# Performance work log

Measured on AMD Instinct MI355X. Metric: run time of the kernel, lower is better.

The kernel has to match this reference:

```python
import jax, jax.numpy as jnp
import numpy as np

ANG_Y, ANG_X = 3, 3
ST = ANG_Y * ANG_X
K = 9                      # square kernel
OH, OW = 128, 128          # output_size
IN_C, OUT_C = 3, 3
H, W = 384, 384
B = 4


def setup_inputs() -> dict:
    key = jax.random.key(0)
    k_lf, = jax.random.split(key, 1)
    lf = jax.random.uniform(k_lf, (B, ST, IN_C, H, W), dtype=jnp.float32)
    # Learned locally-connected weights: one (out_c, in_c, OH, OW, K*K) tensor
    # per angular position, initialized as the center-tap identity (as in __init__).
    weights = jnp.zeros((ST, OUT_C, IN_C, OH, OW, K * K), dtype=jnp.float32)
    center = (K * K) // 2
    ch = jnp.arange(IN_C)
    weights = weights.at[:, ch, ch, :, :, center].set(1.0)
    biases = jnp.zeros((ST, OUT_C, OH, OW), dtype=jnp.float32)
    return {"lf": lf, "weights": weights, "biases": biases}


def reference(lf, weights, biases):
    b, st, c, h, w = lf.shape
    dh, dw = ANG_Y, ANG_X  # unfold stride
    # Padding exactly as in linear_filter
    pad_x = (OW - 1) * ANG_X + (K - w)
    pad_right = pad_x // 2
    pad_left = pad_x - pad_right
    pad_y = (OH - 1) * ANG_Y + (K - h)
    pad_bottom = pad_y // 2
    pad_top = pad_y - pad_bottom
    padded = jnp.pad(
        lf, ((0, 0), (0, 0), (0, 0), (pad_top, pad_bottom), (pad_left, pad_right))
    )
    # Extract K x K windows with stride (dh, dw), vectorized over batch and
    # all angular positions at once (replaces the triple Python loop).
    rows = jnp.arange(OH) * dh          # (OH,)
    cols = jnp.arange(OW) * dw          # (OW,)
    koff = jnp.arange(K)                # (K,)
    p = padded[:, :, :, rows[:, None] + koff[None, :], :]          # (b,st,c,OH,K,Wp)
    p = p[:, :, :, :, :, cols[:, None] + koff[None, :]]            # (b,st,c,OH,K,OW,K)
    p = p.transpose(0, 1, 2, 3, 5, 4, 6).reshape(b, st, c, OH, OW, K * K)
    # Locally-connected (unshared-weight) conv: per-angular, per-pixel weights.
    out = jnp.einsum("bsihwk,soihwk->bsohw", p, weights) + biases[None]
    return jnp.clip(out, 0.0, 1.0)
```

## Files before the change

### kernel.cpp

```cpp
#include <hip/hip_runtime.h>


#define ST 9
#define INC 3
#define OUTC 3
#define OHH 128
#define OWW 128
#define KDIM 9
#define KK 81
#define HH 384
#define WW 384
#define HWSZ (HH*WW)
#define WQ 32
#define SLICE (WQ*KK)

typedef float f32x4 __attribute__((ext_vector_type(4)));
struct __attribute__((packed, aligned(4))) U4 { f32x4 v; };

__device__ __forceinline__ void gll16(const float* g, float* l) {
  __builtin_amdgcn_global_load_lds((const __attribute__((address_space(1))) void*)g,
                                   (__attribute__((address_space(3))) void*)l, 16, 0, 0);
}

__global__ __launch_bounds__(128) void lf_filter_kernel(
    const float* __restrict__ lf, const float* __restrict__ wts,
    const float* __restrict__ bias, float* __restrict__ out)
{
  __shared__ __align__(16) float ldsW[OUTC][SLICE];

  const int t   = threadIdx.x;
  const int wl  = t & 31;
  const int b   = t >> 5;
  const int bid = blockIdx.x;
  const int wq  = bid & 3;
  const int h   = (bid >> 2) & 127;
  const int s   = bid >> 9;
  const int w   = wq*WQ + wl;
  const int xbase = 3*w - 3;
  const int ybase = 3*h - 3;

  const int  base  = xbase < 0 ? 0 : (xbase > WW-KDIM ? WW-KDIM : xbase);
  const bool s_neg = (xbase < base);
  const bool s_pos = (xbase > base);

  const float* lfb = lf + (size_t)(b*ST + s)*INC*HWSZ;
  const int wu = (t & ~63) * 4;

  float acc[OUTC] = {0.f, 0.f, 0.f};

  #pragma unroll 1
  for (int i = 0; i < INC; ++i) {
    __syncthreads();

    #pragma unroll
    for (int o = 0; o < OUTC; ++o) {
      const float* wsrc = wts + ((size_t)(((s*OUTC + o)*INC + i)*OHH + h)*OWW + wq*WQ)*KK;
      float* dst = ldsW[o];
      #pragma unroll
      for (int j = 0; j < 5; ++j)
        gll16(wsrc + (size_t)(j*128 + t)*4, dst + j*512 + wu);
      if (t < 8)
        gll16(wsrc + (size_t)(640 + t)*4, dst + 2560 + wu);
    }
    __syncthreads();

    const float* lfr = lfb + (size_t)i*HWSZ;
    const int wb = wl*KK;
    #pragma unroll 1
    for (int ky = 0; ky < KDIM; ++ky) {
      const int y = ybase + ky;
      if ((unsigned)y < (unsigned)HH) {
        const float* rp = lfr + (size_t)y*WW + base;
        const f32x4 va = reinterpret_cast<const U4*>(rp)->v;
        const f32x4 vb = reinterpret_cast<const U4*>(rp + 4)->v;
        const float rc = rp[8];
        const float raw[KDIM] = {va.x, va.y, va.z, va.w, vb.x, vb.y, vb.z, vb.w, rc};
        float lv[KDIM];
        #pragma unroll
        for (int kx = 0; kx < KDIM; ++kx) {
          const float nv = (kx >= 3) ? raw[kx-3] : 0.f;
          const float pv = (kx <= 5) ? raw[kx+3] : 0.f;
          lv[kx] = s_neg ? nv : (s_pos ? pv : raw[kx]);
        }
        #pragma unroll
        for (int o = 0; o < OUTC; ++o) {
          const float* wrow = &ldsW[o][wb + ky*KDIM];
          float a = acc[o];
          #pragma unroll
          for (int kx = 0; kx < KDIM; ++kx)
            a = fmaf(lv[kx], wrow[kx], a);
          acc[o] = a;
        }
      }
    }
  }

  #pragma unroll
  for (int o = 0; o < OUTC; ++o) {
    const float bv = bias[((s*OUTC + o)*OHH + h)*OWW + w];
    float r = acc[o] + bv;
    r = r < 0.f ? 0.f : (r > 1.f ? 1.f : r);
    out[(((size_t)(b*ST + s)*OUTC + o)*OHH + h)*OWW + w] = r;
  }
}

extern "C" void kernel_launch(void* const* d_in, const int* in_sizes, int n_in,
                              void* d_out, int out_size, void* d_ws, size_t ws_size,
                              hipStream_t stream) {
  const float* lf   = (const float*)d_in[0];
  const float* wts  = (const float*)d_in[1];
  const float* bias = (const float*)d_in[2];
  float* out = (float*)d_out;
  dim3 grid(ST * OHH * 4);
  dim3 block(128);
  hipLaunchKernelGGL(lf_filter_kernel, grid, block, 0, stream, lf, wts, bias, out);
}
```

Before: 116.7 us.

## Read per-pixel weights directly from global memory instead of staging through LDS

```diff
diff --git a/kernel.cpp b/kernel.cpp
--- a/kernel.cpp
+++ b/kernel.cpp
@@ -11,31 +11,23 @@
 #define HH 384
 #define WW 384
 #define HWSZ (HH*WW)
-#define WQ 32
-#define SLICE (WQ*KK)
 
 typedef float f32x4 __attribute__((ext_vector_type(4)));
 struct __attribute__((packed, aligned(4))) U4 { f32x4 v; };
-
-__device__ __forceinline__ void gll16(const float* g, float* l) {
-  __builtin_amdgcn_global_load_lds((const __attribute__((address_space(1))) void*)g,
-                                   (__attribute__((address_space(3))) void*)l, 16, 0, 0);
-}
 
 __global__ __launch_bounds__(128) void lf_filter_kernel(
     const float* __restrict__ lf, const float* __restrict__ wts,
     const float* __restrict__ bias, float* __restrict__ out)
 {
-  __shared__ __align__(16) float ldsW[OUTC][SLICE];
-
   const int t   = threadIdx.x;
-  const int wl  = t & 31;
-  const int b   = t >> 5;
+  const int wl  = t & 15;
+  const int b   = (t >> 4) & 3;
+  const int wh  = t >> 6;
   const int bid = blockIdx.x;
-  const int wq  = bid & 3;
+  const int wg  = bid & 3;
   const int h   = (bid >> 2) & 127;
   const int s   = bid >> 9;
-  const int w   = wq*WQ + wl;
+  const int w   = wg*32 + wh*16 + wl;
   const int xbase = 3*w - 3;
   const int ybase = 3*h - 3;
 
@@ -43,29 +35,14 @@
   const bool s_neg = (xbase < base);
   const bool s_pos = (xbase > base);
 
-  const float* lfb = lf + (size_t)(b*ST + s)*INC*HWSZ;
-  const int wu = (t & ~63) * 4;
+  const float* lfb  = lf + (size_t)(b*ST + s)*INC*HWSZ;
+  const size_t wofs = (size_t)w*KK;
 
   float acc[OUTC] = {0.f, 0.f, 0.f};
 
   #pragma unroll 1
   for (int i = 0; i < INC; ++i) {
-    __syncthreads();
-
-    #pragma unroll
-    for (int o = 0; o < OUTC; ++o) {
-      const float* wsrc = wts + ((size_t)(((s*OUTC + o)*INC + i)*OHH + h)*OWW + wq*WQ)*KK;
-      float* dst = ldsW[o];
-      #pragma unroll
-      for (int j = 0; j < 5; ++j)
-        gll16(wsrc + (size_t)(j*128 + t)*4, dst + j*512 + wu);
-      if (t < 8)
-        gll16(wsrc + (size_t)(640 + t)*4, dst + 2560 + wu);
-    }
-    __syncthreads();
-
     const float* lfr = lfb + (size_t)i*HWSZ;
-    const int wb = wl*KK;
     #pragma unroll 1
     for (int ky = 0; ky < KDIM; ++ky) {
       const int y = ybase + ky;
@@ -74,21 +51,31 @@
         const f32x4 va = reinterpret_cast<const U4*>(rp)->v;
         const f32x4 vb = reinterpret_cast<const U4*>(rp + 4)->v;
         const float rc = rp[8];
-        const float raw[KDIM] = {va.x, va.y, va.z, va.w, vb.x, vb.y, vb.z, vb.w, rc};
+        const float raw9[KDIM] = {va.x, va.y, va.z, va.w, vb.x, vb.y, vb.z, vb.w, rc};
         float lv[KDIM];
         #pragma unroll
         for (int kx = 0; kx < KDIM; ++kx) {
-          const float nv = (kx >= 3) ? raw[kx-3] : 0.f;
-          const float pv = (kx <= 5) ? raw[kx+3] : 0.f;
-          lv[kx] = s_neg ? nv : (s_pos ? pv : raw[kx]);
+          const float nv = (kx >= 3) ? raw9[kx-3] : 0.f;
+          const float pv = (kx <= 5) ? raw9[kx+3] : 0.f;
+          lv[kx] = s_neg ? nv : (s_pos ? pv : raw9[kx]);
         }
         #pragma unroll
         for (int o = 0; o < OUTC; ++o) {
-          const float* wrow = &ldsW[o][wb + ky*KDIM];
+          const float* wr = wts + ((size_t)(((s*OUTC + o)*INC + i)*OHH + h))*OWW*KK
+                              + wofs + ky*KDIM;
+          const f32x4 wa = reinterpret_cast<const U4*>(wr)->v;
+          const f32x4 wb2 = reinterpret_cast<const U4*>(wr + 4)->v;
+          const float wc = wr[8];
           float a = acc[o];
-          #pragma unroll
-          for (int kx = 0; kx < KDIM; ++kx)
-            a = fmaf(lv[kx], wrow[kx], a);
+          a = fmaf(lv[0], wa.x, a);
+          a = fmaf(lv[1], wa.y, a);
+          a = fmaf(lv[2], wa.z, a);
+          a = fmaf(lv[3], wa.w, a);
+          a = fmaf(lv[4], wb2.x, a);
+          a = fmaf(lv[5], wb2.y, a);
+          a = fmaf(lv[6], wb2.z, a);
+          a = fmaf(lv[7], wb2.w, a);
+          a = fmaf(lv[8], wc, a);
           acc[o] = a;
         }
       }
```

After: 262.8 us. 2.25x slower.
